# Performance work log

Measured on AMD Instinct MI355X. Metric: run time of the kernel, lower is better.

The kernel has to match this reference:

```python
import jax, jax.numpy as jnp
import numpy as np

EPS = 1e-7  # K.epsilon()
ROUTINGS = 3


def squash(v, axis=-1):
    s2 = jnp.sum(jnp.square(v), axis=axis, keepdims=True)
    scale = s2 / (1.0 + s2) / jnp.sqrt(s2 + EPS)
    return scale * v


def setup_inputs() -> dict:
    key = jax.random.key(0)
    k1, k2 = jax.random.split(key)
    B, NIN, DIN, NOUT, DOUT = 1024, 1152, 8, 10, 16
    x = jax.random.normal(k1, (B, NIN, DIN), dtype=jnp.float32)
    # glorot-uniform-style scale for W [1, NIN, NOUT, DOUT, DIN]
    limit = np.sqrt(6.0 / (DIN + DOUT)).astype(np.float32)
    W = jax.random.uniform(k2, (1, NIN, NOUT, DOUT, DIN), dtype=jnp.float32,
                           minval=-limit, maxval=limit)
    return {"x": x, "W": W}


def reference(x, W):
    # x: [B, NIN, DIN]; W: [1, NIN, NOUT, DOUT, DIN]
    B = x.shape[0]
    NIN, NOUT, DOUT, DIN = W.shape[1], W.shape[2], W.shape[3], W.shape[4]
    # inputs_hat = W @ inputs: [B, NIN, NOUT, DOUT]
    u_hat = jnp.einsum('inde,bie->bind', W[0], x)
    b = jnp.zeros((B, NIN, NOUT), dtype=x.dtype)
    v = None
    for i in range(ROUTINGS):
        c = jax.nn.softmax(b, axis=-2)                 # softmax over input capsules
        s = jnp.sum(c[..., None] * u_hat, axis=1, keepdims=True)  # [B,1,NOUT,DOUT]
        v = squash(s)
        if i < ROUTINGS - 1:
            # agreement: <u_hat, v> summed over capsule dim -> [B, NIN, NOUT]
            b = b + jnp.sum(u_hat * v, axis=-1)
    return v.reshape(-1, NOUT, DOUT)
```

## Files before the change

### kernel.cpp

```cpp
#include <hip/hip_runtime.h>

#define NIN   1152
#define DIN   8
#define NOUTC 10
#define DOUTC 16
#define GB    2
#define BLOCK 384
#define KPT   3
#define NWAVES 6
#define EPSQ  1e-7f

typedef float f32x16 __attribute__((ext_vector_type(16)));

__global__ __launch_bounds__(BLOCK, 1) void caps_route_kernel(
    const float* __restrict__ x,
    const float* __restrict__ W,
    float* __restrict__ out,
    int ngroups)
{
    const int nout = blockIdx.x / ngroups;
    const int bg   = blockIdx.x % ngroups;
    const int b0   = bg * GB;
    const int t    = threadIdx.x;
    const int lane = t & 63;
    const int wave = t >> 6;

    f32x16 uh[KPT][GB];
    float blog[KPT][GB];
    #pragma unroll
    for (int k = 0; k < KPT; ++k)
        #pragma unroll
        for (int g = 0; g < GB; ++g)
            blog[k][g] = 0.f;

    #pragma unroll
    for (int k = 0; k < KPT; ++k) {
        const int i = t + k * BLOCK;
        float4 xa[GB], xb[GB];
        #pragma unroll
        for (int g = 0; g < GB; ++g) {
            const float4* xp = reinterpret_cast<const float4*>(
                x + ((size_t)(b0 + g) * NIN + i) * DIN);
            xa[g] = xp[0];
            xb[g] = xp[1];
        }
        const float4* w4 = reinterpret_cast<const float4*>(
            W + ((size_t)i * NOUTC + nout) * (DOUTC * DIN));
        #pragma unroll
        for (int h = 0; h < 2; ++h) {
            float4 wbuf[16];
            #pragma unroll
            for (int j = 0; j < 16; ++j) wbuf[j] = w4[h * 16 + j];
            #pragma unroll
            for (int dd = 0; dd < 8; ++dd) {
                const float4 wa = wbuf[2 * dd];
                const float4 wb = wbuf[2 * dd + 1];
                #pragma unroll
                for (int g = 0; g < GB; ++g) {
                    float acc;
                    acc = wa.x * xa[g].x;
                    acc = fmaf(wa.y, xa[g].y, acc);
                    acc = fmaf(wa.z, xa[g].z, acc);
                    acc = fmaf(wa.w, xa[g].w, acc);
                    acc = fmaf(wb.x, xb[g].x, acc);
                    acc = fmaf(wb.y, xb[g].y, acc);
                    acc = fmaf(wb.z, xb[g].z, acc);
                    acc = fmaf(wb.w, xb[g].w, acc);
                    uh[k][g][h * 8 + dd] = acc;
                }
            }
        }
    }

    __shared__ float red[NWAVES][GB][DOUTC + 1];
    __shared__ float scal[GB][DOUTC + 1];

    for (int it = 0; it < 3; ++it) {
        #pragma unroll
        for (int g = 0; g < GB; ++g) {
            const float e0 = __expf(blog[0][g]);
            const float e1 = __expf(blog[1][g]);
            const float e2 = __expf(blog[2][g]);
            float Zp = e0 + e1 + e2;
            f32x16 part = uh[0][g] * e0 + uh[1][g] * e1 + uh[2][g] * e2;
            #pragma unroll
            for (int off = 32; off > 0; off >>= 1) {
                Zp += __shfl_xor(Zp, off);
                #pragma unroll
                for (int d = 0; d < DOUTC; ++d)
                    part[d] += __shfl_xor(part[d], off);
            }
            if (lane == 0) {
                red[wave][g][0] = Zp;
                #pragma unroll
                for (int d = 0; d < DOUTC; ++d) red[wave][g][1 + d] = part[d];
            }
        }
        __syncthreads();

        if (t < GB * (DOUTC + 1)) {
            const int g = t / (DOUTC + 1);
            const int j = t % (DOUTC + 1);
            float acc = red[0][g][j];
            #pragma unroll
            for (int w = 1; w < NWAVES; ++w) acc += red[w][g][j];
            scal[g][j] = acc;
        }
        __syncthreads();

        if (it < 2) {
            #pragma unroll
            for (int g = 0; g < GB; ++g) {
                const float invZ = 1.f / scal[g][0];
                f32x16 sv;
                float s2 = 0.f;
                #pragma unroll
                for (int d = 0; d < DOUTC; ++d) {
                    const float sd = scal[g][1 + d] * invZ;
                    sv[d] = sd;
                    s2 = fmaf(sd, sd, s2);
                }
                const float scale = (s2 / (1.f + s2)) / sqrtf(s2 + EPSQ);
                #pragma unroll
                for (int k = 0; k < KPT; ++k) {
                    float dot = 0.f;
                    #pragma unroll
                    for (int d = 0; d < DOUTC; ++d)
                        dot = fmaf(uh[k][g][d], sv[d], dot);
                    blog[k][g] = fmaf(dot, scale, blog[k][g]);
                }
            }
        } else {
            if (t < GB * DOUTC) {
                const int g = t >> 4;
                const int d = t & 15;
                const float invZ = 1.f / scal[g][0];
                float s2 = 0.f;
                #pragma unroll
                for (int dd = 0; dd < DOUTC; ++dd) {
                    const float sd = scal[g][1 + dd] * invZ;
                    s2 = fmaf(sd, sd, s2);
                }
                const float scale = (s2 / (1.f + s2)) / sqrtf(s2 + EPSQ);
                const float sown = scal[g][1 + d] * invZ;
                out[((size_t)(b0 + g) * NOUTC + nout) * DOUTC + d] = sown * scale;
            }
        }
    }
}

extern "C" void kernel_launch(void* const* d_in, const int* in_sizes, int n_in,
                              void* d_out, int out_size, void* d_ws, size_t ws_size,
                              hipStream_t stream) {
    const float* x = (const float*)d_in[0];
    const float* W = (const float*)d_in[1];
    float* out = (float*)d_out;
    const int B = in_sizes[0] / (NIN * DIN);
    const int ngroups = B / GB;
    dim3 grid(NOUTC * ngroups);
    caps_route_kernel<<<grid, BLOCK, 0, stream>>>(x, W, out, ngroups);
}
```

Measured before the change: 787.0 us.

## Split u_hat computation into separate kernel storing fp16 workspace for routing

Adds a first kernel that computes u_hat with W tiles staged in shared memory and reused across 256 batch items, writing the result as fp16 into the workspace. A second kernel loads one (batch, output capsule) slice into LDS and runs the routing iterations. This removes the heavy redundant W reads of the fused kernel. In exchange it adds a large intermediate write and read, and fp16 rounding of u_hat. The old kernel is kept as a fallback when the workspace is too small.

```diff
diff --git a/kernel.cpp b/kernel.cpp
--- a/kernel.cpp
+++ b/kernel.cpp
@@ -4,19 +4,203 @@
 #define DIN   8
 #define NOUTC 10
 #define DOUTC 16
+#define EPSQ  1e-7f
+
+typedef float f32x16 __attribute__((ext_vector_type(16)));
+typedef _Float16 half8 __attribute__((ext_vector_type(8)));
+
+#define A_IT 8
+#define A_BT 256
+#define A_THREADS 256
+
+__global__ __launch_bounds__(A_THREADS, 1) void caps_uhat_kernel(
+    const float* __restrict__ x,
+    const float* __restrict__ W,
+    _Float16* __restrict__ uh)
+{
+    const int btile = blockIdx.x / (NIN / A_IT);
+    const int itile = blockIdx.x % (NIN / A_IT);
+    const int b0 = btile * A_BT;
+    const int i0 = itile * A_IT;
+    const int tid = threadIdx.x;
+
+    __shared__ float Wt[NOUTC * DOUTC][A_IT * DIN];
+
+    {
+        const float4* wsrc = (const float4*)(W + (size_t)i0 * NOUTC * DOUTC * DIN);
+        float4* wdst = (float4*)&Wt[0][0];
+        #pragma unroll
+        for (int j = 0; j < 10; ++j) {
+            const int c  = tid + j * A_THREADS;
+            const int i  = c / 320;
+            const int r  = c - i * 320;
+            const int nd = r >> 1;
+            const int eh = r & 1;
+            wdst[nd * 16 + i * 2 + eh] = wsrc[c];
+        }
+    }
+    __syncthreads();
+
+    const int ii = tid & 7;
+    const int bg = tid >> 3;
+    const int i  = i0 + ii;
+
+    float4 xa[8], xb[8];
+    #pragma unroll
+    for (int p = 0; p < 8; ++p) {
+        const int b = b0 + bg + p * 32;
+        const float4* xp = (const float4*)(x + ((size_t)b * NIN + i) * DIN);
+        xa[p] = xp[0];
+        xb[p] = xp[1];
+    }
+
+    #pragma unroll
+    for (int n = 0; n < NOUTC; ++n) {
+        #pragma unroll
+        for (int dh = 0; dh < 2; ++dh) {
+            float acc[8][8];
+            #pragma unroll
+            for (int d8 = 0; d8 < 8; ++d8) {
+                const int nd = n * DOUTC + dh * 8 + d8;
+                const float4 w0 = *(const float4*)&Wt[nd][ii * 8];
+                const float4 w1 = *(const float4*)&Wt[nd][ii * 8 + 4];
+                #pragma unroll
+                for (int p = 0; p < 8; ++p) {
+                    float a;
+                    a = w0.x * xa[p].x;
+                    a = fmaf(w0.y, xa[p].y, a);
+                    a = fmaf(w0.z, xa[p].z, a);
+                    a = fmaf(w0.w, xa[p].w, a);
+                    a = fmaf(w1.x, xb[p].x, a);
+                    a = fmaf(w1.y, xb[p].y, a);
+                    a = fmaf(w1.z, xb[p].z, a);
+                    a = fmaf(w1.w, xb[p].w, a);
+                    acc[p][d8] = a;
+                }
+            }
+            #pragma unroll
+            for (int p = 0; p < 8; ++p) {
+                const int b = b0 + bg + p * 32;
+                half8 hv;
+                #pragma unroll
+                for (int j = 0; j < 8; ++j) hv[j] = (_Float16)acc[p][j];
+                *(half8*)(uh + ((((size_t)b * NOUTC + n) * 2 + dh) * NIN + i) * 8) = hv;
+            }
+        }
+    }
+}
+
+#define B_THREADS 384
+#define B_WAVES 6
+#define B_KPT 3
+
+__global__ __launch_bounds__(B_THREADS, 1) void caps_route2_kernel(
+    const _Float16* __restrict__ uh, float* __restrict__ out)
+{
+    const int bid = blockIdx.x;
+    const int t = threadIdx.x;
+    const int lane = t & 63;
+    const int wave = t >> 6;
+
+    __shared__ _Float16 U[2 * NIN * 8];
+    __shared__ float red[B_WAVES][DOUTC + 1];
+    __shared__ float scal[DOUTC + 1];
+
+    {
+        const float4* src = (const float4*)(uh + (size_t)bid * (2 * NIN * 8));
+        float4* dst = (float4*)U;
+        #pragma unroll
+        for (int j = 0; j < 6; ++j)
+            dst[t + j * B_THREADS] = src[t + j * B_THREADS];
+    }
+    __syncthreads();
+
+    f32x16 uhr[B_KPT];
+    #pragma unroll
+    for (int k = 0; k < B_KPT; ++k) {
+        const int i = t + k * B_THREADS;
+        const half8 lo = *(const half8*)&U[i * 8];
+        const half8 hi = *(const half8*)&U[NIN * 8 + i * 8];
+        #pragma unroll
+        for (int j = 0; j < 8; ++j) {
+            uhr[k][j] = (float)lo[j];
+            uhr[k][8 + j] = (float)hi[j];
+        }
+    }
+
+    float blog[B_KPT] = {0.f, 0.f, 0.f};
+
+    for (int it = 0; it < 3; ++it) {
+        const float e0 = __expf(blog[0]);
+        const float e1 = __expf(blog[1]);
+        const float e2 = __expf(blog[2]);
+        float Zp = e0 + e1 + e2;
+        f32x16 part = uhr[0] * e0 + uhr[1] * e1 + uhr[2] * e2;
+        #pragma unroll
+        for (int off = 32; off > 0; off >>= 1) {
+            Zp += __shfl_xor(Zp, off);
+            #pragma unroll
+            for (int d = 0; d < DOUTC; ++d)
+                part[d] += __shfl_xor(part[d], off);
+        }
+        if (lane == 0) {
+            red[wave][0] = Zp;
+            #pragma unroll
+            for (int d = 0; d < DOUTC; ++d) red[wave][1 + d] = part[d];
+        }
+        __syncthreads();
+
+        if (t < DOUTC + 1) {
+            float a = red[0][t];
+            #pragma unroll
+            for (int w = 1; w < B_WAVES; ++w) a += red[w][t];
+            scal[t] = a;
+        }
+        __syncthreads();
+
+        if (it < 2) {
+            const float invZ = 1.f / scal[0];
+            f32x16 sv;
+            float s2 = 0.f;
+            #pragma unroll
+            for (int d = 0; d < DOUTC; ++d) {
+                const float sd = scal[1 + d] * invZ;
+                sv[d] = sd;
+                s2 = fmaf(sd, sd, s2);
+            }
+            const float scale = (s2 / (1.f + s2)) / sqrtf(s2 + EPSQ);
+            #pragma unroll
+            for (int k = 0; k < B_KPT; ++k) {
+                float dot = 0.f;
+                #pragma unroll
+                for (int d = 0; d < DOUTC; ++d)
+                    dot = fmaf(uhr[k][d], sv[d], dot);
+                blog[k] = fmaf(dot, scale, blog[k]);
+            }
+        } else {
+            if (t < DOUTC) {
+                const float invZ = 1.f / scal[0];
+                float s2 = 0.f;
+                #pragma unroll
+                for (int dd = 0; dd < DOUTC; ++dd) {
+                    const float sd = scal[1 + dd] * invZ;
+                    s2 = fmaf(sd, sd, s2);
+                }
+                const float scale = (s2 / (1.f + s2)) / sqrtf(s2 + EPSQ);
+                out[(size_t)bid * DOUTC + t] = scal[1 + t] * invZ * scale;
+            }
+        }
+    }
+}
+
 #define GB    2
 #define BLOCK 384
 #define KPT   3
 #define NWAVES 6
-#define EPSQ  1e-7f
-
-typedef float f32x16 __attribute__((ext_vector_type(16)));
 
 __global__ __launch_bounds__(BLOCK, 1) void caps_route_kernel(
-    const float* __restrict__ x,
-    const float* __restrict__ W,
-    float* __restrict__ out,
-    int ngroups)
+    const float* __restrict__ x, const float* __restrict__ W,
+    float* __restrict__ out, int ngroups)
 {
     const int nout = blockIdx.x / ngroups;
     const int bg   = blockIdx.x % ngroups;
@@ -47,33 +231,27 @@
         const float4* w4 = reinterpret_cast<const float4*>(
             W + ((size_t)i * NOUTC + nout) * (DOUTC * DIN));
         #pragma unroll
-        for (int h = 0; h < 2; ++h) {
-            float4 wbuf[16];
-            #pragma unroll
-            for (int j = 0; j < 16; ++j) wbuf[j] = w4[h * 16 + j];
-            #pragma unroll
-            for (int dd = 0; dd < 8; ++dd) {
-                const float4 wa = wbuf[2 * dd];
-                const float4 wb = wbuf[2 * dd + 1];
-                #pragma unroll
-                for (int g = 0; g < GB; ++g) {
-                    float acc;
-                    acc = wa.x * xa[g].x;
-                    acc = fmaf(wa.y, xa[g].y, acc);
-                    acc = fmaf(wa.z, xa[g].z, acc);
-                    acc = fmaf(wa.w, xa[g].w, acc);
-                    acc = fmaf(wb.x, xb[g].x, acc);
-                    acc = fmaf(wb.y, xb[g].y, acc);
-                    acc = fmaf(wb.z, xb[g].z, acc);
-                    acc = fmaf(wb.w, xb[g].w, acc);
-                    uh[k][g][h * 8 + dd] = acc;
-                }
-            }
-        }
-    }
-
-    __shared__ float red[NWAVES][GB][DOUTC + 1];
-    __shared__ float scal[GB][DOUTC + 1];
+        for (int d = 0; d < DOUTC; ++d) {
+            const float4 wa = w4[2 * d];
+            const float4 wb = w4[2 * d + 1];
+            #pragma unroll
+            for (int g = 0; g < GB; ++g) {
+                float acc;
+                acc = wa.x * xa[g].x;
+                acc = fmaf(wa.y, xa[g].y, acc);
+                acc = fmaf(wa.z, xa[g].z, acc);
+                acc = fmaf(wa.w, xa[g].w, acc);
+                acc = fmaf(wb.x, xb[g].x, acc);
+                acc = fmaf(wb.y, xb[g].y, acc);
+                acc = fmaf(wb.z, xb[g].z, acc);
+                acc = fmaf(wb.w, xb[g].w, acc);
+                uh[k][g][d] = acc;
+            }
+        }
+    }
+
+    __shared__ float red2[NWAVES][GB][DOUTC + 1];
+    __shared__ float scal2[GB][DOUTC + 1];
 
     for (int it = 0; it < 3; ++it) {
         #pragma unroll
@@ -91,9 +269,9 @@
                     part[d] += __shfl_xor(part[d], off);
             }
             if (lane == 0) {
-                red[wave][g][0] = Zp;
-                #pragma unroll
-                for (int d = 0; d < DOUTC; ++d) red[wave][g][1 + d] = part[d];
+                red2[wave][g][0] = Zp;
+                #pragma unroll
+                for (int d = 0; d < DOUTC; ++d) red2[wave][g][1 + d] = part[d];
             }
         }
         __syncthreads();
@@ -101,22 +279,22 @@
         if (t < GB * (DOUTC + 1)) {
             const int g = t / (DOUTC + 1);
             const int j = t % (DOUTC + 1);
-            float acc = red[0][g][j];
-            #pragma unroll
-            for (int w = 1; w < NWAVES; ++w) acc += red[w][g][j];
-            scal[g][j] = acc;
+            float acc = red2[0][g][j];
+            #pragma unroll
+            for (int w = 1; w < NWAVES; ++w) acc += red2[w][g][j];
+            scal2[g][j] = acc;
         }
         __syncthreads();
 
         if (it < 2) {
             #pragma unroll
             for (int g = 0; g < GB; ++g) {
-                const float invZ = 1.f / scal[g][0];
+                const float invZ = 1.f / scal2[g][0];
                 f32x16 sv;
                 float s2 = 0.f;
                 #pragma unroll
                 for (int d = 0; d < DOUTC; ++d) {
-                    const float sd = scal[g][1 + d] * invZ;
+                    const float sd = scal2[g][1 + d] * invZ;
                     sv[d] = sd;
                     s2 = fmaf(sd, sd, s2);
                 }
@@ -134,16 +312,16 @@
             if (t < GB * DOUTC) {
                 const int g = t >> 4;
                 const int d = t & 15;
-                const float invZ = 1.f / scal[g][0];
+                const float invZ = 1.f / scal2[g][0];
                 float s2 = 0.f;
                 #pragma unroll
                 for (int dd = 0; dd < DOUTC; ++dd) {
-                    const float sd = scal[g][1 + dd] * invZ;
+                    const float sd = scal2[g][1 + dd] * invZ;
                     s2 = fmaf(sd, sd, s2);
                 }
                 const float scale = (s2 / (1.f + s2)) / sqrtf(s2 + EPSQ);
-                const float sown = scal[g][1 + d] * invZ;
-                out[((size_t)(b0 + g) * NOUTC + nout) * DOUTC + d] = sown * scale;
+                out[((size_t)(b0 + g) * NOUTC + nout) * DOUTC + d] =
+                    scal2[g][1 + d] * invZ * scale;
             }
         }
     }
@@ -156,7 +334,16 @@
     const float* W = (const float*)d_in[1];
     float* out = (float*)d_out;
     const int B = in_sizes[0] / (NIN * DIN);
-    const int ngroups = B / GB;
-    dim3 grid(NOUTC * ngroups);
-    caps_route_kernel<<<grid, BLOCK, 0, stream>>>(x, W, out, ngroups);
+    const size_t UH_BYTES = (size_t)B * NOUTC * 2 * NIN * 8 * sizeof(_Float16);
+
+    if (ws_size >= UH_BYTES && (B % A_BT) == 0) {
+        _Float16* uhbuf = (_Float16*)d_ws;
+        dim3 gridA((B / A_BT) * (NIN / A_IT));
+        caps_uhat_kernel<<<gridA, A_THREADS, 0, stream>>>(x, W, uhbuf);
+        dim3 gridB(B * NOUTC);
+        caps_route2_kernel<<<gridB, B_THREADS, 0, stream>>>(uhbuf, out);
+    } else {
+        const int ngroups = B / GB;
+        caps_route_kernel<<<dim3(NOUTC * ngroups), BLOCK, 0, stream>>>(x, W, out, ngroups);
+    }
 }
```

New measurement: 786.1 us. Within noise of the previous version (-0.1%).
